# Kernel optimization log

Measured on AMD Instinct MI355X. Metric: run time of the kernel, lower is better.

Reference implementation:

```python
import jax, jax.numpy as jnp
import numpy as np

N, E, D, H, C, K = 100000, 1250000, 64, 64, 40, 2


def setup_inputs() -> dict:
    key = jax.random.key(0)
    ks = jax.random.split(key, 10)
    s_in = 1.0 / np.sqrt(D)
    s_cat = 1.0 / np.sqrt(H * (K + 1))
    return {
        "x": jax.random.normal(ks[0], (N, D), jnp.float32),
        "edge_index": jax.random.randint(ks[1], (2, E), 0, N, dtype=jnp.int64),
        "W_ego": jax.random.normal(ks[2], (D, H), jnp.float32) * s_in,
        "b_ego": jnp.zeros((H,), jnp.float32),
        "W_conv": jax.random.normal(ks[3], (K, D, H), jnp.float32) * s_in,
        "b_conv": jnp.zeros((K, H), jnp.float32),
        "W_cls": jax.random.normal(ks[4], (H * (K + 1), C), jnp.float32) * s_cat,
        "b_cls": jnp.zeros((C,), jnp.float32),
    }


def _gcn_norm(edge_index, n):
    # PyG GCNConv default: add self-loops, symmetric normalization.
    row = jnp.concatenate([edge_index[0], jnp.arange(n, dtype=edge_index.dtype)])
    col = jnp.concatenate([edge_index[1], jnp.arange(n, dtype=edge_index.dtype)])
    deg = jax.ops.segment_sum(jnp.ones_like(col, dtype=jnp.float32), col, num_segments=n)
    dis = jnp.where(deg > 0, jax.lax.rsqrt(jnp.maximum(deg, 1.0)), 0.0)
    norm = dis[row] * dis[col]  # [E+N]
    return row, col, norm


def _gcn_conv(h, W, b, row, col, norm, n):
    hw = h @ W                                   # [N, H] transform first (cheap d)
    msg = norm[:, None] * hw[row]                # gather + scale, [E+N, H]
    agg = jax.ops.segment_sum(msg, col, num_segments=n)  # scatter-add to targets
    return agg + b


def reference(x, edge_index, W_ego, b_ego, W_conv, b_conv, W_cls, b_cls):
    n = x.shape[0]
    row, col, norm = _gcn_norm(edge_index, n)
    parts = [jax.nn.relu(x @ W_ego + b_ego)]
    h = x
    for k in range(K):
        h = jax.nn.relu(_gcn_conv(h, W_conv[k], b_conv[k], row, col, norm, n))
        parts.append(h)
    out = jnp.concatenate(parts, axis=-1)        # [N, H*(K+1)]
    # dropout is identity at inference (training=False)
    return out @ W_cls + b_cls
```

## Files before the change

kernel.cpp:

```cpp
#include <hip/hip_runtime.h>

using u16 = unsigned short;
using u32 = unsigned int;
using short8 = __attribute__((ext_vector_type(8))) short;
using f32x4  = __attribute__((ext_vector_type(4))) float;

static inline int cdiv(long long a, long long b) { return (int)((a + b - 1) / b); }

__device__ __forceinline__ u16 f2bf(float x) {
    u32 u = __builtin_bit_cast(u32, x);
    u += 0x7fffu + ((u >> 16) & 1u);
    return (u16)(u >> 16);
}
__device__ __forceinline__ float bf2f(u16 h) {
    u32 u = ((u32)h) << 16;
    return __builtin_bit_cast(float, u);
}

#define BKT_SH 10
#define BKT_MASK ((1 << BKT_SH) - 1)
#define CHUNK 4096

__global__ __launch_bounds__(256) void k_bhist(const int* __restrict__ ei,
                                               int* __restrict__ bcntg, int E) {
    __shared__ int lb[128];
    if (threadIdx.x < 128) lb[threadIdx.x] = 0;
    __syncthreads();
    const int eb = blockIdx.x * CHUNK;
#pragma unroll
    for (int k = 0; k < 16; ++k) {
        int e = eb + k * 256 + threadIdx.x;
        if (e < E) atomicAdd(&lb[ei[E + e] >> BKT_SH], 1);
    }
    __syncthreads();
    if (threadIdx.x < 128 && lb[threadIdx.x] > 0)
        atomicAdd(&bcntg[threadIdx.x], lb[threadIdx.x]);
}

__global__ __launch_bounds__(128) void k_bscan(const int* __restrict__ bcntg,
                                               int* __restrict__ bbase,
                                               int* __restrict__ bcursor, int NB) {
    __shared__ int s[128];
    int t = threadIdx.x;
    int v = (t < NB) ? bcntg[t] : 0;
    s[t] = v;
    __syncthreads();
    for (int st = 1; st < 128; st <<= 1) {
        int add = (t >= st) ? s[t - st] : 0;
        __syncthreads();
        s[t] += add;
        __syncthreads();
    }
    int excl = s[t] - v;
    if (t < NB) { bbase[t] = excl; bcursor[t] = excl; }
    if (t == NB - 1) bbase[NB] = excl + v;
}

__global__ __launch_bounds__(256) void k_passA(const int* __restrict__ ei,
                                               int* __restrict__ bcursor,
                                               u32* __restrict__ sta, int E) {
    __shared__ int lcnt[128];
    __shared__ int lcur[128];
    if (threadIdx.x < 128) lcnt[threadIdx.x] = 0;
    __syncthreads();
    const int eb = blockIdx.x * CHUNK;
    int er[16], ec[16];
#pragma unroll
    for (int k = 0; k < 16; ++k) {
        int e = eb + k * 256 + threadIdx.x;
        if (e < E) {
            er[k] = ei[e];
            ec[k] = ei[E + e];
            atomicAdd(&lcnt[ec[k] >> BKT_SH], 1);
        } else {
            ec[k] = -1;
        }
    }
    __syncthreads();
    if (threadIdx.x < 128)
        lcur[threadIdx.x] = lcnt[threadIdx.x] > 0
                          ? atomicAdd(&bcursor[threadIdx.x], lcnt[threadIdx.x]) : 0;
    __syncthreads();
#pragma unroll
    for (int k = 0; k < 16; ++k) {
        if (ec[k] >= 0) {
            int pos = atomicAdd(&lcur[ec[k] >> BKT_SH], 1);
            sta[pos] = ((u32)(ec[k] & BKT_MASK) << 17) | (u32)er[k];
        }
    }
}

__global__ __launch_bounds__(256) void k_passB(const u32* __restrict__ sta,
                                               const int* __restrict__ bbase,
                                               int* __restrict__ indptr,
                                               float* __restrict__ dis,
                                               int* __restrict__ rows,
                                               int N, int NB) {
    __shared__ int lcnt[1024];
    __shared__ int cur[1024];
    __shared__ int ps[256];
    const int b = blockIdx.x;
    const int t = threadIdx.x;
    const int base = b << BKT_SH;
    const int e0 = bbase[b], e1 = bbase[b + 1];

#pragma unroll
    for (int k = 0; k < 4; ++k) lcnt[k * 256 + t] = 0;
    __syncthreads();
    for (int e = e0 + t; e < e1; e += 256)
        atomicAdd(&lcnt[sta[e] >> 17], 1);
    __syncthreads();

    int a0 = lcnt[t * 4 + 0], a1 = lcnt[t * 4 + 1];
    int a2 = lcnt[t * 4 + 2], a3 = lcnt[t * 4 + 3];
    int sum = a0 + a1 + a2 + a3;
    ps[t] = sum;
    __syncthreads();
    for (int st = 1; st < 256; st <<= 1) {
        int add = (t >= st) ? ps[t - st] : 0;
        __syncthreads();
        ps[t] += add;
        __syncthreads();
    }
    int ex = e0 + ps[t] - sum;
    int exs[4] = {ex, ex + a0, ex + a0 + a1, ex + a0 + a1 + a2};
    int cnts[4] = {a0, a1, a2, a3};
#pragma unroll
    for (int k = 0; k < 4; ++k) {
        int j = t * 4 + k;
        cur[j] = exs[k];
        int node = base + j;
        if (node < N) {
            indptr[node] = exs[k];
            dis[node] = rsqrtf((float)cnts[k] + 1.0f);
        }
    }
    if (b == NB - 1 && t == 0) indptr[N] = bbase[NB];
    __syncthreads();

    for (int e = e0 + t; e < e1; e += 256) {
        u32 v = sta[e];
        int pos = atomicAdd(&cur[v >> 17], 1);
        rows[pos] = (int)(v & 0x1FFFF);
    }
}

__global__ __launch_bounds__(256) void k_prep(const float* __restrict__ Wego,
                                              const float* __restrict__ Wconv,
                                              const float* __restrict__ Wcls,
                                              u16* __restrict__ WTin,
                                              u16* __restrict__ WT1,
                                              u16* __restrict__ WcatT) {
    int t = blockIdx.x * 256 + threadIdx.x;
    if (t < 128 * 64) {
        int seg = t >> 6, d = t & 63;
        float v = (seg < 64) ? Wconv[d * 64 + seg] : Wego[d * 64 + (seg - 64)];
        WTin[t] = f2bf(v);
    } else if (t < 128 * 64 + 64 * 64) {
        int u = t - 128 * 64;
        int c = u >> 6, d = u & 63;
        WT1[u] = f2bf(Wconv[64 * 64 + d * 64 + c]);
    } else if (t < 128 * 64 + 64 * 64 + 48 * 192) {
        int u = t - (128 * 64 + 64 * 64);
        int c = u / 192, d = u - c * 192;
        WcatT[u] = f2bf(c < 40 ? Wcls[d * 40 + c] : 0.f);
    }
}

__global__ __launch_bounds__(256) void k_in(const float* __restrict__ x,
                                            const u16* __restrict__ WTin,
                                            const float* __restrict__ dis,
                                            const float* __restrict__ bego,
                                            u16* __restrict__ hws,
                                            u16* __restrict__ hall, int N) {
    const int wid = (blockIdx.x * 256 + threadIdx.x) >> 6;
    const int l = threadIdx.x & 63;
    if (wid * 16 >= N) return;
    const int lr = l & 15;
    const int lk = l >> 4;

    int r_ld = wid * 16 + lr;
    if (r_ld >= N) r_ld = N - 1;
    const float* xrow = x + (size_t)r_ld * 64 + lk * 8;
    float4 u0 = *(const float4*)(xrow);
    float4 u1 = *(const float4*)(xrow + 4);
    float4 u2 = *(const float4*)(xrow + 32);
    float4 u3 = *(const float4*)(xrow + 36);
    short8 a0, a1;
    a0[0] = (short)f2bf(u0.x); a0[1] = (short)f2bf(u0.y);
    a0[2] = (short)f2bf(u0.z); a0[3] = (short)f2bf(u0.w);
    a0[4] = (short)f2bf(u1.x); a0[5] = (short)f2bf(u1.y);
    a0[6] = (short)f2bf(u1.z); a0[7] = (short)f2bf(u1.w);
    a1[0] = (short)f2bf(u2.x); a1[1] = (short)f2bf(u2.y);
    a1[2] = (short)f2bf(u2.z); a1[3] = (short)f2bf(u2.w);
    a1[4] = (short)f2bf(u3.x); a1[5] = (short)f2bf(u3.y);
    a1[6] = (short)f2bf(u3.z); a1[7] = (short)f2bf(u3.w);

    float dvals[4];
#pragma unroll
    for (int rg = 0; rg < 4; ++rg) {
        int r = wid * 16 + lk * 4 + rg;
        dvals[rg] = dis[r < N ? r : N - 1];
    }

    for (int ct = 0; ct < 8; ++ct) {
        const u16* wrow = WTin + ((size_t)(ct * 16 + lr)) * 64 + lk * 8;
        short8 b0 = *(const short8*)wrow;
        short8 b1 = *(const short8*)(wrow + 32);
        f32x4 acc = {0.f, 0.f, 0.f, 0.f};
        acc = __builtin_amdgcn_mfma_f32_16x16x32_bf16(a0, b0, acc, 0, 0, 0);
        acc = __builtin_amdgcn_mfma_f32_16x16x32_bf16(a1, b1, acc, 0, 0, 0);
        const int col = ct * 16 + lr;
        if (col < 64) {
#pragma unroll
            for (int rg = 0; rg < 4; ++rg) {
                int r = wid * 16 + lk * 4 + rg;
                if (r < N) hws[(size_t)r * 64 + col] = f2bf(dvals[rg] * acc[rg]);
            }
        } else {
            float be = bego[col - 64];
#pragma unroll
            for (int rg = 0; rg < 4; ++rg) {
                int r = wid * 16 + lk * 4 + rg;
                if (r < N) hall[(size_t)r * 192 + (col - 64)] = f2bf(fmaxf(acc[rg] + be, 0.f));
            }
        }
    }
}

__global__ __launch_bounds__(512) void k_gather(const int* __restrict__ indptr,
                                                const int* __restrict__ rows,
                                                const float* __restrict__ dis,
                                                const float* __restrict__ bconv,
                                                const u16* __restrict__ hws_in,
                                                u16* __restrict__ hdst, int N) {
    const int w = threadIdx.x >> 6;
    const int f = threadIdx.x & 63;
    const int i = blockIdx.x * 8 + w;
    if (i >= N) return;

    float acc = bf2f(hws_in[(size_t)i * 64 + f]);
    int p0 = __builtin_amdgcn_readfirstlane(indptr[i]);
    int p1 = __builtin_amdgcn_readfirstlane(indptr[i + 1]);
    int p = p0;
    for (; p + 8 <= p1; p += 8) {
        int r0 = rows[p + 0], r1 = rows[p + 1], r2 = rows[p + 2], r3 = rows[p + 3];
        int r4 = rows[p + 4], r5 = rows[p + 5], r6 = rows[p + 6], r7 = rows[p + 7];
        u16 v0 = hws_in[(size_t)r0 * 64 + f];
        u16 v1 = hws_in[(size_t)r1 * 64 + f];
        u16 v2 = hws_in[(size_t)r2 * 64 + f];
        u16 v3 = hws_in[(size_t)r3 * 64 + f];
        u16 v4 = hws_in[(size_t)r4 * 64 + f];
        u16 v5 = hws_in[(size_t)r5 * 64 + f];
        u16 v6 = hws_in[(size_t)r6 * 64 + f];
        u16 v7 = hws_in[(size_t)r7 * 64 + f];
        acc += ((bf2f(v0) + bf2f(v1)) + (bf2f(v2) + bf2f(v3))) +
               ((bf2f(v4) + bf2f(v5)) + (bf2f(v6) + bf2f(v7)));
    }
    for (; p + 4 <= p1; p += 4) {
        int r0 = rows[p + 0], r1 = rows[p + 1], r2 = rows[p + 2], r3 = rows[p + 3];
        u16 v0 = hws_in[(size_t)r0 * 64 + f];
        u16 v1 = hws_in[(size_t)r1 * 64 + f];
        u16 v2 = hws_in[(size_t)r2 * 64 + f];
        u16 v3 = hws_in[(size_t)r3 * 64 + f];
        acc += (bf2f(v0) + bf2f(v1)) + (bf2f(v2) + bf2f(v3));
    }
    for (; p < p1; ++p) acc += bf2f(hws_in[(size_t)rows[p] * 64 + f]);

    float hv = fmaxf(fmaf(dis[i], acc, bconv[f]), 0.0f);
    hdst[(size_t)i * 192 + f] = f2bf(hv);
}

__global__ __launch_bounds__(256) void k_next1(const u16* __restrict__ hall,
                                               const u16* __restrict__ WT1,
                                               const float* __restrict__ dis,
                                               u16* __restrict__ hws, int N) {
    const int wid = (blockIdx.x * 256 + threadIdx.x) >> 6;
    const int l = threadIdx.x & 63;
    if (wid * 16 >= N) return;
    const int lr = l & 15;
    const int lk = l >> 4;

    int r_ld = wid * 16 + lr;
    if (r_ld >= N) r_ld = N - 1;
    const u16* arow = hall + (size_t)r_ld * 192 + 64 + lk * 8;
    short8 a0 = *(const short8*)arow;
    short8 a1 = *(const short8*)(arow + 32);

    float dvals[4];
#pragma unroll
    for (int rg = 0; rg < 4; ++rg) {
        int r = wid * 16 + lk * 4 + rg;
        dvals[rg] = dis[r < N ? r : N - 1];
    }

    for (int ct = 0; ct < 4; ++ct) {
        const u16* wrow = WT1 + ((size_t)(ct * 16 + lr)) * 64 + lk * 8;
        short8 b0 = *(const short8*)wrow;
        short8 b1 = *(const short8*)(wrow + 32);
        f32x4 acc = {0.f, 0.f, 0.f, 0.f};
        acc = __builtin_amdgcn_mfma_f32_16x16x32_bf16(a0, b0, acc, 0, 0, 0);
        acc = __builtin_amdgcn_mfma_f32_16x16x32_bf16(a1, b1, acc, 0, 0, 0);
        const int col = ct * 16 + lr;
#pragma unroll
        for (int rg = 0; rg < 4; ++rg) {
            int r = wid * 16 + lk * 4 + rg;
            if (r < N) hws[(size_t)r * 64 + col] = f2bf(dvals[rg] * acc[rg]);
        }
    }
}

__global__ __launch_bounds__(256) void k_clsall(const u16* __restrict__ hall,
                                                const u16* __restrict__ WcatT,
                                                const float* __restrict__ bcls,
                                                float* __restrict__ out, int N) {
    const int wid = (blockIdx.x * 256 + threadIdx.x) >> 6;
    const int l = threadIdx.x & 63;
    if (wid * 16 >= N) return;
    const int lr = l & 15;
    const int lk = l >> 4;

    int r_ld = wid * 16 + lr;
    if (r_ld >= N) r_ld = N - 1;
    const u16* arow = hall + (size_t)r_ld * 192 + lk * 8;
    short8 a[6];
#pragma unroll
    for (int kt = 0; kt < 6; ++kt) a[kt] = *(const short8*)(arow + kt * 32);

    for (int ct = 0; ct < 3; ++ct) {
        const u16* brow = WcatT + ((size_t)(ct * 16 + lr)) * 192 + lk * 8;
        f32x4 acc = {0.f, 0.f, 0.f, 0.f};
#pragma unroll
        for (int kt = 0; kt < 6; ++kt) {
            short8 b = *(const short8*)(brow + kt * 32);
            acc = __builtin_amdgcn_mfma_f32_16x16x32_bf16(a[kt], b, acc, 0, 0, 0);
        }
        const int col = ct * 16 + lr;
        if (col < 40) {
            float bc = bcls[col];
#pragma unroll
            for (int rg = 0; rg < 4; ++rg) {
                int r = wid * 16 + lk * 4 + rg;
                if (r < N) out[(size_t)r * 40 + col] = bc + acc[rg];
            }
        }
    }
}

extern "C" void kernel_launch(void* const* d_in, const int* in_sizes, int n_in,
                              void* d_out, int out_size, void* d_ws, size_t ws_size,
                              hipStream_t stream) {
    const float* x     = (const float*)d_in[0];
    const int*   ei    = (const int*)d_in[1];
    const float* Wego  = (const float*)d_in[2];
    const float* bego  = (const float*)d_in[3];
    const float* Wconv = (const float*)d_in[4];
    const float* bconv = (const float*)d_in[5];
    const float* Wcls  = (const float*)d_in[6];
    const float* bcls  = (const float*)d_in[7];
    float* out = (float*)d_out;

    const int N = in_sizes[0] / 64;
    const int E = in_sizes[1] / 2;
    const int NB = cdiv(N, 1 << BKT_SH);

    u16* hall   = (u16*)d_ws;
    u32* sta    = (u32*)d_ws;
    u16* hwsbuf = hall + (size_t)N * 192;
    u16* WTin   = hwsbuf + (size_t)N * 64;
    u16* WT1    = WTin + 128 * 64;
    u16* WcatT  = WT1 + 64 * 64;
    float* dis  = (float*)(WcatT + 48 * 192);
    int* indptr  = (int*)(dis + N);
    int* bcntg   = indptr + N + 64;
    int* bbase   = bcntg + 128;
    int* bcursor = bbase + 132;
    int* rows    = bcursor + 128;

    hipMemsetAsync(bcntg, 0, 128 * sizeof(int), stream);

    k_bhist<<<cdiv(E, CHUNK), 256, 0, stream>>>(ei, bcntg, E);
    k_bscan<<<1, 128, 0, stream>>>(bcntg, bbase, bcursor, NB);
    k_passA<<<cdiv(E, CHUNK), 256, 0, stream>>>(ei, bcursor, sta, E);
    k_passB<<<NB, 256, 0, stream>>>(sta, bbase, indptr, dis, rows, N, NB);

    k_prep<<<cdiv(128 * 64 + 64 * 64 + 48 * 192, 256), 256, 0, stream>>>(
        Wego, Wconv, Wcls, WTin, WT1, WcatT);
    const int n_blk16 = cdiv(cdiv(N, 16), 4);
    k_in<<<n_blk16, 256, 0, stream>>>(x, WTin, dis, bego, hwsbuf, hall, N);

    k_gather<<<cdiv(N, 8), 512, 0, stream>>>(indptr, rows, dis, bconv,
                                             hwsbuf, hall + 64, N);
    k_next1<<<n_blk16, 256, 0, stream>>>(hall, WT1, dis, hwsbuf, N);

    k_gather<<<cdiv(N, 8), 512, 0, stream>>>(indptr, rows, dis, bconv + 64,
                                             hwsbuf, hall + 128, N);

    k_clsall<<<n_blk16, 256, 0, stream>>>(hall, WcatT, bcls, out, N);
}
```

Baseline: 215.3 us.

## Fuse gather with following matmuls and merge histogram with weight prep

Fuses each neighbor-gather kernel with the dense matmul that follows it: the first gather now also computes the next-layer transform through shared memory, and the second gather feeds the classifier directly. This removes the k_next1 and k_clsall launches along with the round trip of the last hidden layer through global memory, and shrinks the hall buffer from 192 to 128 columns. The bucket histogram and the weight-prep kernel are merged into one launch that writes per-block partial counts, which removes the memset and global atomics; k_bscan then sums the partials serially. The cost is 1024-thread blocks where only a few waves run the MFMA tail after a block-wide barrier, plus a serial partial-sum loop in the scan.

After: 253.5 us. 1.18x slower.

```diff
diff --git a/kernel.cpp b/kernel.cpp
--- a/kernel.cpp
+++ b/kernel.cpp
@@ -21,28 +21,53 @@
 #define BKT_MASK ((1 << BKT_SH) - 1)
 #define CHUNK 4096
 
-__global__ __launch_bounds__(256) void k_bhist(const int* __restrict__ ei,
-                                               int* __restrict__ bcntg, int E) {
-    __shared__ int lb[128];
-    if (threadIdx.x < 128) lb[threadIdx.x] = 0;
-    __syncthreads();
-    const int eb = blockIdx.x * CHUNK;
-#pragma unroll
-    for (int k = 0; k < 16; ++k) {
-        int e = eb + k * 256 + threadIdx.x;
-        if (e < E) atomicAdd(&lb[ei[E + e] >> BKT_SH], 1);
-    }
-    __syncthreads();
-    if (threadIdx.x < 128 && lb[threadIdx.x] > 0)
-        atomicAdd(&bcntg[threadIdx.x], lb[threadIdx.x]);
-}
-
-__global__ __launch_bounds__(128) void k_bscan(const int* __restrict__ bcntg,
+__global__ __launch_bounds__(256) void k_init(const int* __restrict__ ei,
+                                              int* __restrict__ bpart, int E, int NBH,
+                                              const float* __restrict__ Wego,
+                                              const float* __restrict__ Wconv,
+                                              const float* __restrict__ Wcls,
+                                              u16* __restrict__ WTin,
+                                              u16* __restrict__ WT1,
+                                              u16* __restrict__ WcatT) {
+    if ((int)blockIdx.x < NBH) {
+        __shared__ int lb[128];
+        if (threadIdx.x < 128) lb[threadIdx.x] = 0;
+        __syncthreads();
+        const int eb = blockIdx.x * CHUNK;
+#pragma unroll
+        for (int k = 0; k < 16; ++k) {
+            int e = eb + k * 256 + threadIdx.x;
+            if (e < E) atomicAdd(&lb[ei[E + e] >> BKT_SH], 1);
+        }
+        __syncthreads();
+        if (threadIdx.x < 128)
+            bpart[blockIdx.x * 128 + threadIdx.x] = lb[threadIdx.x];
+    } else {
+        int t = ((int)blockIdx.x - NBH) * 256 + threadIdx.x;
+        if (t < 128 * 64) {
+            int seg = t >> 6, d = t & 63;
+            float v = (seg < 64) ? Wconv[d * 64 + seg] : Wego[d * 64 + (seg - 64)];
+            WTin[t] = f2bf(v);
+        } else if (t < 128 * 64 + 64 * 64) {
+            int u = t - 128 * 64;
+            int c = u >> 6, d = u & 63;
+            WT1[u] = f2bf(Wconv[64 * 64 + d * 64 + c]);
+        } else if (t < 128 * 64 + 64 * 64 + 48 * 192) {
+            int u = t - (128 * 64 + 64 * 64);
+            int c = u / 192, d = u - c * 192;
+            WcatT[u] = f2bf(c < 40 ? Wcls[d * 40 + c] : 0.f);
+        }
+    }
+}
+
+__global__ __launch_bounds__(128) void k_bscan(const int* __restrict__ bpart, int NBH,
                                                int* __restrict__ bbase,
                                                int* __restrict__ bcursor, int NB) {
     __shared__ int s[128];
     int t = threadIdx.x;
-    int v = (t < NB) ? bcntg[t] : 0;
+    int c = 0;
+    for (int b = 0; b < NBH; ++b) c += bpart[b * 128 + t];
+    int v = (t < NB) ? c : 0;
     s[t] = v;
     __syncthreads();
     for (int st = 1; st < 128; st <<= 1) {
@@ -145,33 +170,11 @@
     }
 }
 
-__global__ __launch_bounds__(256) void k_prep(const float* __restrict__ Wego,
-                                              const float* __restrict__ Wconv,
-                                              const float* __restrict__ Wcls,
-                                              u16* __restrict__ WTin,
-                                              u16* __restrict__ WT1,
-                                              u16* __restrict__ WcatT) {
-    int t = blockIdx.x * 256 + threadIdx.x;
-    if (t < 128 * 64) {
-        int seg = t >> 6, d = t & 63;
-        float v = (seg < 64) ? Wconv[d * 64 + seg] : Wego[d * 64 + (seg - 64)];
-        WTin[t] = f2bf(v);
-    } else if (t < 128 * 64 + 64 * 64) {
-        int u = t - 128 * 64;
-        int c = u >> 6, d = u & 63;
-        WT1[u] = f2bf(Wconv[64 * 64 + d * 64 + c]);
-    } else if (t < 128 * 64 + 64 * 64 + 48 * 192) {
-        int u = t - (128 * 64 + 64 * 64);
-        int c = u / 192, d = u - c * 192;
-        WcatT[u] = f2bf(c < 40 ? Wcls[d * 40 + c] : 0.f);
-    }
-}
-
 __global__ __launch_bounds__(256) void k_in(const float* __restrict__ x,
                                             const u16* __restrict__ WTin,
                                             const float* __restrict__ dis,
                                             const float* __restrict__ bego,
-                                            u16* __restrict__ hws,
+                                            u16* __restrict__ hws1,
                                             u16* __restrict__ hall, int N) {
     const int wid = (blockIdx.x * 256 + threadIdx.x) >> 6;
     const int l = threadIdx.x & 63;
@@ -215,30 +218,23 @@
 #pragma unroll
             for (int rg = 0; rg < 4; ++rg) {
                 int r = wid * 16 + lk * 4 + rg;
-                if (r < N) hws[(size_t)r * 64 + col] = f2bf(dvals[rg] * acc[rg]);
+                if (r < N) hws1[(size_t)r * 64 + col] = f2bf(dvals[rg] * acc[rg]);
             }
         } else {
             float be = bego[col - 64];
 #pragma unroll
             for (int rg = 0; rg < 4; ++rg) {
                 int r = wid * 16 + lk * 4 + rg;
-                if (r < N) hall[(size_t)r * 192 + (col - 64)] = f2bf(fmaxf(acc[rg] + be, 0.f));
+                if (r < N) hall[(size_t)r * 128 + (col - 64)] = f2bf(fmaxf(acc[rg] + be, 0.f));
             }
         }
     }
 }
 
-__global__ __launch_bounds__(512) void k_gather(const int* __restrict__ indptr,
-                                                const int* __restrict__ rows,
-                                                const float* __restrict__ dis,
-                                                const float* __restrict__ bconv,
-                                                const u16* __restrict__ hws_in,
-                                                u16* __restrict__ hdst, int N) {
-    const int w = threadIdx.x >> 6;
-    const int f = threadIdx.x & 63;
-    const int i = blockIdx.x * 8 + w;
-    if (i >= N) return;
-
+__device__ __forceinline__ float gather_acc(const int* __restrict__ indptr,
+                                            const int* __restrict__ rows,
+                                            const u16* __restrict__ hws_in,
+                                            int i, int f) {
     float acc = bf2f(hws_in[(size_t)i * 64 + f]);
     int p0 = __builtin_amdgcn_readfirstlane(indptr[i]);
     int p1 = __builtin_amdgcn_readfirstlane(indptr[i + 1]);
@@ -266,81 +262,97 @@
         acc += (bf2f(v0) + bf2f(v1)) + (bf2f(v2) + bf2f(v3));
     }
     for (; p < p1; ++p) acc += bf2f(hws_in[(size_t)rows[p] * 64 + f]);
-
-    float hv = fmaxf(fmaf(dis[i], acc, bconv[f]), 0.0f);
-    hdst[(size_t)i * 192 + f] = f2bf(hv);
-}
-
-__global__ __launch_bounds__(256) void k_next1(const u16* __restrict__ hall,
-                                               const u16* __restrict__ WT1,
-                                               const float* __restrict__ dis,
-                                               u16* __restrict__ hws, int N) {
-    const int wid = (blockIdx.x * 256 + threadIdx.x) >> 6;
-    const int l = threadIdx.x & 63;
-    if (wid * 16 >= N) return;
-    const int lr = l & 15;
-    const int lk = l >> 4;
-
-    int r_ld = wid * 16 + lr;
-    if (r_ld >= N) r_ld = N - 1;
-    const u16* arow = hall + (size_t)r_ld * 192 + 64 + lk * 8;
-    short8 a0 = *(const short8*)arow;
-    short8 a1 = *(const short8*)(arow + 32);
-
-    float dvals[4];
-#pragma unroll
-    for (int rg = 0; rg < 4; ++rg) {
-        int r = wid * 16 + lk * 4 + rg;
-        dvals[rg] = dis[r < N ? r : N - 1];
-    }
-
-    for (int ct = 0; ct < 4; ++ct) {
-        const u16* wrow = WT1 + ((size_t)(ct * 16 + lr)) * 64 + lk * 8;
+    return acc;
+}
+
+__global__ __launch_bounds__(1024) void k_g1(const int* __restrict__ indptr,
+                                             const int* __restrict__ rows,
+                                             const float* __restrict__ dis,
+                                             const float* __restrict__ bconv,
+                                             const u16* __restrict__ hws1,
+                                             const u16* __restrict__ WT1,
+                                             u16* __restrict__ hall,
+                                             u16* __restrict__ hws2, int N) {
+    __shared__ __align__(16) u16 sh[16][64];
+    const int wv = threadIdx.x >> 6;
+    const int f = threadIdx.x & 63;
+    const int i = blockIdx.x * 16 + wv;
+    u16 hv16 = 0;
+    if (i < N) {
+        float acc = gather_acc(indptr, rows, hws1, i, f);
+        float hvf = fmaxf(fmaf(dis[i], acc, bconv[f]), 0.0f);
+        hv16 = f2bf(hvf);
+        hall[(size_t)i * 128 + 64 + f] = hv16;
+    }
+    sh[wv][f] = hv16;
+    __syncthreads();
+
+    if (wv < 4) {
+        const int lr = f & 15, lk = f >> 4;
+        short8 a0 = *(const short8*)&sh[lr][lk * 8];
+        short8 a1 = *(const short8*)&sh[lr][lk * 8 + 32];
+        const u16* wrow = WT1 + ((size_t)(wv * 16 + lr)) * 64 + lk * 8;
         short8 b0 = *(const short8*)wrow;
         short8 b1 = *(const short8*)(wrow + 32);
         f32x4 acc = {0.f, 0.f, 0.f, 0.f};
         acc = __builtin_amdgcn_mfma_f32_16x16x32_bf16(a0, b0, acc, 0, 0, 0);
         acc = __builtin_amdgcn_mfma_f32_16x16x32_bf16(a1, b1, acc, 0, 0, 0);
-        const int col = ct * 16 + lr;
+        const int col = wv * 16 + lr;
 #pragma unroll
         for (int rg = 0; rg < 4; ++rg) {
-            int r = wid * 16 + lk * 4 + rg;
-            if (r < N) hws[(size_t)r * 64 + col] = f2bf(dvals[rg] * acc[rg]);
-        }
-    }
-}
-
-__global__ __launch_bounds__(256) void k_clsall(const u16* __restrict__ hall,
-                                                const u16* __restrict__ WcatT,
-                                                const float* __restrict__ bcls,
-                                                float* __restrict__ out, int N) {
-    const int wid = (blockIdx.x * 256 + threadIdx.x) >> 6;
-    const int l = threadIdx.x & 63;
-    if (wid * 16 >= N) return;
-    const int lr = l & 15;
-    const int lk = l >> 4;
-
-    int r_ld = wid * 16 + lr;
-    if (r_ld >= N) r_ld = N - 1;
-    const u16* arow = hall + (size_t)r_ld * 192 + lk * 8;
-    short8 a[6];
-#pragma unroll
-    for (int kt = 0; kt < 6; ++kt) a[kt] = *(const short8*)(arow + kt * 32);
-
-    for (int ct = 0; ct < 3; ++ct) {
-        const u16* brow = WcatT + ((size_t)(ct * 16 + lr)) * 192 + lk * 8;
+            int r = blockIdx.x * 16 + lk * 4 + rg;
+            if (r < N) hws2[(size_t)r * 64 + col] = f2bf(dis[r] * acc[rg]);
+        }
+    }
+}
+
+__global__ __launch_bounds__(1024) void k_g2(const int* __restrict__ indptr,
+                                             const int* __restrict__ rows,
+                                             const float* __restrict__ dis,
+                                             const float* __restrict__ bconv1,
+                                             const u16* __restrict__ hws2,
+                                             const u16* __restrict__ hall,
+                                             const u16* __restrict__ WcatT,
+                                             const float* __restrict__ bcls,
+                                             float* __restrict__ out, int N) {
+    __shared__ __align__(16) u16 sh[16][64];
+    const int wv = threadIdx.x >> 6;
+    const int f = threadIdx.x & 63;
+    const int i = blockIdx.x * 16 + wv;
+    u16 hv16 = 0;
+    if (i < N) {
+        float acc = gather_acc(indptr, rows, hws2, i, f);
+        float hvf = fmaxf(fmaf(dis[i], acc, bconv1[f]), 0.0f);
+        hv16 = f2bf(hvf);
+    }
+    sh[wv][f] = hv16;
+    __syncthreads();
+
+    if (wv < 3) {
+        const int lr = f & 15, lk = f >> 4;
+        int arow = blockIdx.x * 16 + lr;
+        if (arow >= N) arow = N - 1;
+        const u16* hrow = hall + (size_t)arow * 128 + lk * 8;
+        short8 a[6];
+        a[0] = *(const short8*)(hrow);
+        a[1] = *(const short8*)(hrow + 32);
+        a[2] = *(const short8*)(hrow + 64);
+        a[3] = *(const short8*)(hrow + 96);
+        a[4] = *(const short8*)&sh[lr][lk * 8];
+        a[5] = *(const short8*)&sh[lr][lk * 8 + 32];
+        const u16* brow = WcatT + ((size_t)(wv * 16 + lr)) * 192 + lk * 8;
         f32x4 acc = {0.f, 0.f, 0.f, 0.f};
 #pragma unroll
         for (int kt = 0; kt < 6; ++kt) {
             short8 b = *(const short8*)(brow + kt * 32);
             acc = __builtin_amdgcn_mfma_f32_16x16x32_bf16(a[kt], b, acc, 0, 0, 0);
         }
-        const int col = ct * 16 + lr;
+        const int col = wv * 16 + lr;
         if (col < 40) {
             float bc = bcls[col];
 #pragma unroll
             for (int rg = 0; rg < 4; ++rg) {
-                int r = wid * 16 + lk * 4 + rg;
+                int r = blockIdx.x * 16 + lk * 4 + rg;
                 if (r < N) out[(size_t)r * 40 + col] = bc + acc[rg];
             }
         }
@@ -362,39 +374,34 @@
 
     const int N = in_sizes[0] / 64;
     const int E = in_sizes[1] / 2;
-    const int NB = cdiv(N, 1 << BKT_SH);
-
-    u16* hall   = (u16*)d_ws;
-    u32* sta    = (u32*)d_ws;
-    u16* hwsbuf = hall + (size_t)N * 192;
-    u16* WTin   = hwsbuf + (size_t)N * 64;
-    u16* WT1    = WTin + 128 * 64;
-    u16* WcatT  = WT1 + 64 * 64;
-    float* dis  = (float*)(WcatT + 48 * 192);
+    const int NB  = cdiv(N, 1 << BKT_SH);
+    const int NBH = cdiv(E, CHUNK);
+
+    u16* hall  = (u16*)d_ws;
+    u32* sta   = (u32*)d_ws;
+    u16* hws1  = hall + (size_t)N * 128;
+    u16* hws2  = hws1 + (size_t)N * 64;
+    u16* WTin  = hws2 + (size_t)N * 64;
+    u16* WT1   = WTin + 128 * 64;
+    u16* WcatT = WT1 + 64 * 64;
+    float* dis = (float*)(WcatT + 48 * 192);
     int* indptr  = (int*)(dis + N);
-    int* bcntg   = indptr + N + 64;
-    int* bbase   = bcntg + 128;
+    int* bbase   = indptr + N + 64;
     int* bcursor = bbase + 132;
     int* rows    = bcursor + 128;
-
-    hipMemsetAsync(bcntg, 0, 128 * sizeof(int), stream);
-
-    k_bhist<<<cdiv(E, CHUNK), 256, 0, stream>>>(ei, bcntg, E);
-    k_bscan<<<1, 128, 0, stream>>>(bcntg, bbase, bcursor, NB);
-    k_passA<<<cdiv(E, CHUNK), 256, 0, stream>>>(ei, bcursor, sta, E);
+    int* bpart   = rows + E;
+
+    const int PREP_BLOCKS = cdiv(128 * 64 + 64 * 64 + 48 * 192, 256);
+    k_init<<<NBH + PREP_BLOCKS, 256, 0, stream>>>(ei, bpart, E, NBH,
+                                                  Wego, Wconv, Wcls, WTin, WT1, WcatT);
+    k_bscan<<<1, 128, 0, stream>>>(bpart, NBH, bbase, bcursor, NB);
+    k_passA<<<NBH, 256, 0, stream>>>(ei, bcursor, sta, E);
     k_passB<<<NB, 256, 0, stream>>>(sta, bbase, indptr, dis, rows, N, NB);
 
-    k_prep<<<cdiv(128 * 64 + 64 * 64 + 48 * 192, 256), 256, 0, stream>>>(
-        Wego, Wconv, Wcls, WTin, WT1, WcatT);
-    const int n_blk16 = cdiv(cdiv(N, 16), 4);
-    k_in<<<n_blk16, 256, 0, stream>>>(x, WTin, dis, bego, hwsbuf, hall, N);
-
-    k_gather<<<cdiv(N, 8), 512, 0, stream>>>(indptr, rows, dis, bconv,
-                                             hwsbuf, hall + 64, N);
-    k_next1<<<n_blk16, 256, 0, stream>>>(hall, WT1, dis, hwsbuf, N);
-
-    k_gather<<<cdiv(N, 8), 512, 0, stream>>>(indptr, rows, dis, bconv + 64,
-                                             hwsbuf, hall + 128, N);
-
-    k_clsall<<<n_blk16, 256, 0, stream>>>(hall, WcatT, bcls, out, N);
-}
+    k_in<<<cdiv(cdiv(N, 16), 4), 256, 0, stream>>>(x, WTin, dis, bego, hws1, hall, N);
+
+    k_g1<<<cdiv(N, 16), 1024, 0, stream>>>(indptr, rows, dis, bconv,
+                                           hws1, WT1, hall, hws2, N);
+    k_g2<<<cdiv(N, 16), 1024, 0, stream>>>(indptr, rows, dis, bconv + 64,
+                                           hws2, hall, WcatT, bcls, out, N);
+}
```
